# Kernel optimization log

Hardware: AMD Instinct MI355X
Metric: run time of the kernel (lower is better)

The kernel has to match this reference:

```python
import jax, jax.numpy as jnp
import numpy as np

INTERVAL = 0.02

def setup_inputs() -> dict:
    key = jax.random.key(0)
    ks = jax.random.split(key, 10)
    B, N, D, F = 8, 256, 64, 64
    return {
        "rbf_0": jax.random.normal(ks[0], (B, N, N, D), jnp.float32),
        "rbf_d": jax.random.normal(ks[1], (B, N, N, D), jnp.float32),
        "Q0_w": jax.random.normal(ks[2], (F, D), jnp.float32) * 0.1,
        "Q0_b": jax.random.normal(ks[3], (F,), jnp.float32) * 0.1,
        "Q_w": jax.random.normal(ks[4], (F, D), jnp.float32) * 0.1,
        "Q_b": jax.random.normal(ks[5], (F,), jnp.float32) * 0.1,
        "R0_w": jax.random.normal(ks[6], (F, D), jnp.float32) * 0.1,
        "R0_b": jax.random.normal(ks[7], (F,), jnp.float32) * 0.1,
        "R_w": jax.random.normal(ks[8], (F, D), jnp.float32) * 0.1,
        "R_b": jax.random.normal(ks[9], (F,), jnp.float32) * 0.1,
    }

def _linear(x, w, b):
    # x: [..., D], w: [F, D], b: [F] -> [..., F]
    return jnp.einsum('...d,fd->...f', x, w) + b

def reference(rbf_0, rbf_d, Q0_w, Q0_b, Q_w, Q_b, R0_w, R0_b, R_w, R_b):
    q_0 = _linear(rbf_0, Q0_w, Q0_b)   # [B, N, N, F]
    q = _linear(rbf_d, Q_w, Q_b)       # [B, N, N, F]
    r_0 = _linear(rbf_0, R0_w, R0_b)   # [B, N, N, F]
    r = _linear(rbf_d, R_w, R_b)       # [B, N, N, F]
    # 3-index correlator: contract over i and f
    C = jnp.einsum('bnif,bijf->bnj', q_0 * q, r_0 * r) * INTERVAL
    return C
```

## Files before the change

kernel.cpp:

```cpp
#include <hip/hip_runtime.h>
#include <hip/hip_bf16.h>


typedef __bf16 bf16x8 __attribute__((ext_vector_type(8)));
typedef float  f32x4  __attribute__((ext_vector_type(4)));
typedef int    i32x4  __attribute__((ext_vector_type(4)));
typedef unsigned short u16;
typedef u16    u16x8  __attribute__((ext_vector_type(8)));

static __device__ __forceinline__ __bf16 f2bf(float x) {
  union { __hip_bfloat16 h; __bf16 b; } u;
  u.h = __float2bfloat16(x);
  return u.b;
}
static __device__ __forceinline__ u16 f2bfu(float x) {
  union { __hip_bfloat16 h; u16 s; } u;
  u.h = __float2bfloat16(x);
  return u.s;
}
static __device__ __forceinline__ float bfu2f(u16 s) {
  union { unsigned int u; float f; } v;
  v.u = ((unsigned int)s) << 16;
  return v.f;
}
static __device__ __forceinline__ void gload16(const float* gsrc, float* ldst) {
  __builtin_amdgcn_global_load_lds(
      (const __attribute__((address_space(1))) void*)gsrc,
      (__attribute__((address_space(3))) void*)ldst, 16, 0, 0);
}

__global__ __launch_bounds__(256, 3) void k_phase1(
    const float* __restrict__ rbf0, const float* __restrict__ rbfd,
    const float* __restrict__ Q0w, const float* __restrict__ Q0b,
    const float* __restrict__ Qw,  const float* __restrict__ Qb,
    const float* __restrict__ R0w, const float* __restrict__ R0b,
    const float* __restrict__ Rw,  const float* __restrict__ Rb,
    u16* __restrict__ Aout, u16* __restrict__ Bout)
{
  __shared__ __align__(16) float lds[3][2][2048];

  const int tid  = threadIdx.x;
  const int lane = tid & 63;
  const int wave = tid >> 6;
  const int fr   = lane & 15;
  const int kg   = lane >> 4;
  const int role = wave >> 1;
  const int s    = wave & 1;

  const float* W0 = role ? R0w : Q0w;
  const float* W1 = role ? Rw  : Qw;
  const float* B0 = role ? R0b : Q0b;
  const float* B1 = role ? Rb  : Qb;
  u16* __restrict__ Out = role ? Bout : Aout;

  bf16x8 wf0[2][4], wf1[2][4];
#pragma unroll
  for (int kt = 0; kt < 2; ++kt)
#pragma unroll
    for (int ft = 0; ft < 4; ++ft) {
      const float* p0 = W0 + (ft * 16 + fr) * 64 + kt * 32 + kg * 8;
      const float* p1 = W1 + (ft * 16 + fr) * 64 + kt * 32 + kg * 8;
      f32x4 a = *(const f32x4*)p0, b = *(const f32x4*)(p0 + 4);
      f32x4 c = *(const f32x4*)p1, d = *(const f32x4*)(p1 + 4);
      bf16x8 w0v, w1v;
#pragma unroll
      for (int j = 0; j < 4; ++j) {
        w0v[j] = f2bf(a[j]); w0v[j + 4] = f2bf(b[j]);
        w1v[j] = f2bf(c[j]); w1v[j + 4] = f2bf(d[j]);
      }
      wf0[kt][ft] = w0v; wf1[kt][ft] = w1v;
    }

  u16x8 pb0[2], pb1[2];
#pragma unroll
  for (int ft = 0; ft < 4; ++ft)
#pragma unroll
    for (int r = 0; r < 4; ++r) {
      int idx = ft * 4 + r;
      pb0[idx >> 3][idx & 7] = f2bfu(B0[ft * 16 + kg * 4 + r]);
      pb1[idx >> 3][idx & 7] = f2bfu(B1[ft * 16 + kg * 4 + r]);
    }

  const int g0 = tid, g1 = 256 + tid;
  const int c0 = ((g0 >> 4) << 4) | ((g0 & 15) ^ ((g0 >> 4) & 15));
  const int c1 = ((g1 >> 4) << 4) | ((g1 & 15) ^ ((g1 >> 4) & 15));
  const int f0 = c0 * 4, f1 = c1 * 4;
  const int d0 = wave * 256, d1 = (wave + 4) * 256;

  const int bt0 = blockIdx.x;

#define S1_ISSUE(IT, SET)                                              \
  {                                                                    \
    const float* b0_ = rbf0 + (size_t)(bt0 + (IT) * 2048) * 2048;      \
    const float* b1_ = rbfd + (size_t)(bt0 + (IT) * 2048) * 2048;      \
    gload16(b0_ + f0, &lds[SET][0][d0]);                               \
    gload16(b0_ + f1, &lds[SET][0][d1]);                               \
    gload16(b1_ + f0, &lds[SET][1][d0]);                               \
    gload16(b1_ + f1, &lds[SET][1][d1]);                               \
  }

#define S1_COMPUTE(IT, SET)                                            \
  {                                                                    \
    const int row = s * 16 + fr;                     \
    f32x4 ra[4], rb[4];                                                \
    _Pragma("unroll")                                                  \
    for (int kt = 0; kt < 2; ++kt)                                     \
      _Pragma("unroll")                                                \
      for (int h = 0; h < 2; ++h) {                                    \
        int c = kt * 8 + kg * 2 + h;                                   \
        int chunk = (row << 4) | (c ^ fr);                             \
        ra[kt * 2 + h] = *(const f32x4*)&lds[SET][0][chunk * 4];       \
        rb[kt * 2 + h] = *(const f32x4*)&lds[SET][1][chunk * 4];       \
      }                                                                \
    bf16x8 x0f[2], xdf[2];                                             \
    _Pragma("unroll")                                                  \
    for (int kt = 0; kt < 2; ++kt)                                     \
      _Pragma("unroll")                                                \
      for (int j = 0; j < 4; ++j) {                                    \
        x0f[kt][j]     = f2bf(ra[kt * 2][j]);                          \
        x0f[kt][j + 4] = f2bf(ra[kt * 2 + 1][j]);                      \
        xdf[kt][j]     = f2bf(rb[kt * 2][j]);                          \
        xdf[kt][j + 4] = f2bf(rb[kt * 2 + 1][j]);                      \
      }                                                                \
    f32x4 acc0[4], acc1[4];                                            \
    _Pragma("unroll")                                                  \
    for (int ft = 0; ft < 4; ++ft)                                     \
      _Pragma("unroll")                                                \
      for (int r = 0; r < 4; ++r) {                                    \
        int idx = ft * 4 + r;                                          \
        acc0[ft][r] = bfu2f(pb0[idx >> 3][idx & 7]);                   \
        acc1[ft][r] = bfu2f(pb1[idx >> 3][idx & 7]);                   \
      }                                                                \
    _Pragma("unroll")                                                  \
    for (int kt = 0; kt < 2; ++kt)                                     \
      _Pragma("unroll")                                                \
      for (int ft = 0; ft < 4; ++ft) {                                 \
        acc0[ft] = __builtin_amdgcn_mfma_f32_16x16x32_bf16(            \
            wf0[kt][ft], x0f[kt], acc0[ft], 0, 0, 0);                  \
        acc1[ft] = __builtin_amdgcn_mfma_f32_16x16x32_bf16(            \
            wf1[kt][ft], xdf[kt], acc1[ft], 0, 0, 0);                  \
      }                                                                \
    u16x8 o0, o1;                                                      \
    _Pragma("unroll")                                                  \
    for (int ft = 0; ft < 4; ++ft)                                     \
      _Pragma("unroll")                                                \
      for (int r = 0; r < 4; ++r) {                                    \
        int idx = ft * 4 + r;                                          \
        float v = acc0[ft][r] * acc1[ft][r];                           \
        if (idx < 8) o0[idx & 7] = f2bfu(v); else o1[idx & 7] = f2bfu(v); \
      }                                                                \
    u16* dst = Out + ((size_t)((bt0 + (IT) * 2048) * 32 + s * 16 + fr)) * 64 + kg * 16; \
    *(u16x8*)dst       = o0;                                           \
    *(u16x8*)(dst + 8) = o1;                                           \
  }

#define S1_ITER(IT, NWAIT, DO_ISSUE)                                   \
  {                                                                    \
    if (DO_ISSUE) S1_ISSUE((IT) + 2, ((IT) + 2) % 3);                  \
    asm volatile("s_waitcnt vmcnt(" #NWAIT ")" ::: "memory");          \
    __builtin_amdgcn_s_barrier();                                      \
    __builtin_amdgcn_sched_barrier(0);                                 \
    S1_COMPUTE(IT, (IT) % 3);                                          \
    asm volatile("s_waitcnt lgkmcnt(0)" ::: "memory");                 \
    __builtin_amdgcn_s_barrier();                                      \
    __builtin_amdgcn_sched_barrier(0);                                 \
  }

  S1_ISSUE(0, 0);
  S1_ISSUE(1, 1);

  S1_ITER(0,  8, 1);
  S1_ITER(1, 10, 1);
  S1_ITER(2, 12, 1);
  S1_ITER(3, 12, 1);
  S1_ITER(4, 12, 1);
  S1_ITER(5, 12, 1);
  S1_ITER(6,  8, 0);
  S1_ITER(7,  4, 0);

#undef S1_ITER
#undef S1_COMPUTE
#undef S1_ISSUE
}

__global__ __launch_bounds__(256, 2) void k_phase2(
    const u16* __restrict__ A, const u16* __restrict__ Bm,
    float* __restrict__ C)
{
  __shared__ __align__(16) u16 Alds[128 * 64];
  __shared__ __align__(16) u16 Blds[128 * 64];

  const int tid  = threadIdx.x;
  const int lane = tid & 63;
  const int wave = tid >> 6;
  const int fr   = lane & 15;
  const int kg   = lane >> 4;

  const int bid = blockIdx.x;
  const int kc = bid & 15;
  const int jt = (bid >> 4) & 1;
  const int nt = (bid >> 5) & 1;
  const int b  = bid >> 6;
  const int n0 = nt * 128, j0 = jt * 128;
  const int wr = wave >> 1, wc = wave & 1;

  const u16* Ab = A  + (size_t)b * 4194304;
  const u16* Bb = Bm + (size_t)b * 4194304;

  f32x4 acc[4][4];
#pragma unroll
  for (int mt = 0; mt < 4; ++mt)
#pragma unroll
    for (int nn = 0; nn < 4; ++nn) {
      acc[mt][nn][0] = 0.f; acc[mt][nn][1] = 0.f; acc[mt][nn][2] = 0.f; acc[mt][nn][3] = 0.f;
    }

  for (int ii = 0; ii < 16; ++ii) {
    const int i = kc * 16 + ii;

    i32x4 va[4], vb[4];
#pragma unroll
    for (int rep = 0; rep < 4; ++rep) {
      int c = tid + rep * 256;
      int row = c >> 3, ch = c & 7;
      va[rep] = *(const i32x4*)(Ab + (size_t)(n0 + row) * 16384 + (size_t)i * 64 + ch * 8);
      vb[rep] = *(const i32x4*)(Bb + (size_t)i * 16384 + (size_t)(j0 + row) * 64 + ch * 8);
    }
    __syncthreads();
#pragma unroll
    for (int rep = 0; rep < 4; ++rep) {
      int c = tid + rep * 256;
      int row = c >> 3, ch = c & 7;
      int sw = ch ^ (row & 7);
      *(i32x4*)&Alds[row * 64 + sw * 8] = va[rep];
      *(i32x4*)&Blds[row * 64 + sw * 8] = vb[rep];
    }
    __syncthreads();

#pragma unroll
    for (int ks = 0; ks < 2; ++ks) {
      bf16x8 af[4], bfv[4];
#pragma unroll
      for (int mt = 0; mt < 4; ++mt) {
        int row = wr * 64 + mt * 16 + fr;
        int sw = (ks * 4 + kg) ^ (row & 7);
        af[mt] = *(const bf16x8*)&Alds[row * 64 + sw * 8];
      }
#pragma unroll
      for (int nn = 0; nn < 4; ++nn) {
        int row = wc * 64 + nn * 16 + fr;
        int sw = (ks * 4 + kg) ^ (row & 7);
        bfv[nn] = *(const bf16x8*)&Blds[row * 64 + sw * 8];
      }
#pragma unroll
      for (int mt = 0; mt < 4; ++mt)
#pragma unroll
        for (int nn = 0; nn < 4; ++nn)
          acc[mt][nn] = __builtin_amdgcn_mfma_f32_16x16x32_bf16(af[mt], bfv[nn], acc[mt][nn], 0, 0, 0);
    }
  }

  float* Cb = C + ((size_t)b << 16);
#pragma unroll
  for (int mt = 0; mt < 4; ++mt)
#pragma unroll
    for (int nn = 0; nn < 4; ++nn)
#pragma unroll
      for (int r = 0; r < 4; ++r) {
        int n = n0 + wr * 64 + mt * 16 + kg * 4 + r;
        int j = j0 + wc * 64 + nn * 16 + fr;
        atomicAdd(&Cb[n * 256 + j], acc[mt][nn][r] * 0.02f);
      }
}

extern "C" void kernel_launch(void* const* d_in, const int* in_sizes, int n_in,
                              void* d_out, int out_size, void* d_ws, size_t ws_size,
                              hipStream_t stream)
{
  const float* rbf0 = (const float*)d_in[0];
  const float* rbfd = (const float*)d_in[1];
  const float* Q0w  = (const float*)d_in[2];
  const float* Q0b  = (const float*)d_in[3];
  const float* Qw   = (const float*)d_in[4];
  const float* Qb   = (const float*)d_in[5];
  const float* R0w  = (const float*)d_in[6];
  const float* R0b  = (const float*)d_in[7];
  const float* Rw   = (const float*)d_in[8];
  const float* Rb   = (const float*)d_in[9];
  float* out = (float*)d_out;

  u16* Abuf = (u16*)d_ws;
  u16* Bbuf = Abuf + (size_t)33554432;

  hipMemsetAsync(d_out, 0, (size_t)out_size * sizeof(float), stream);
  hipLaunchKernelGGL(k_phase1, dim3(2048), dim3(256), 0, stream,
                     rbf0, rbfd, Q0w, Q0b, Qw, Qb, R0w, R0b, Rw, Rb, Abuf, Bbuf);
  hipLaunchKernelGGL(k_phase2, dim3(512), dim3(256), 0, stream, Abuf, Bbuf, out);
}
```

Measured before the change: 142.1 us.

## Give each wave its own row tile computing all four projections, drop block barriers

Phase 1 now assigns each wave an independent 16-row tile and has it compute all four linear projections (Q0, Q, R0, R) from a per-wave double-buffered LDS staging area. Previously the four waves split the work by role, shared a block-wide triple buffer and needed s_barrier synchronisation. This removes block barriers and lets each wave reuse its loaded rbf tile for both the Q and R products. In exchange every wave holds all four weight sets in registers, which raises register pressure, so occupancy drops to 2 blocks per SIMD and the grid halves to 1024 blocks with shallower prefetch.

Measured after the change: 247.6 us. 1.74x slower.

```diff
diff --git a/kernel.cpp b/kernel.cpp
--- a/kernel.cpp
+++ b/kernel.cpp
@@ -29,7 +29,7 @@
       (__attribute__((address_space(3))) void*)ldst, 16, 0, 0);
 }
 
-__global__ __launch_bounds__(256, 3) void k_phase1(
+__global__ __launch_bounds__(256, 2) void k_phase1(
     const float* __restrict__ rbf0, const float* __restrict__ rbfd,
     const float* __restrict__ Q0w, const float* __restrict__ Q0b,
     const float* __restrict__ Qw,  const float* __restrict__ Qb,
@@ -37,80 +37,79 @@
     const float* __restrict__ Rw,  const float* __restrict__ Rb,
     u16* __restrict__ Aout, u16* __restrict__ Bout)
 {
-  __shared__ __align__(16) float lds[3][2][2048];
+  __shared__ __align__(16) float plds[4][2][2][1024];
 
   const int tid  = threadIdx.x;
   const int lane = tid & 63;
   const int wave = tid >> 6;
   const int fr   = lane & 15;
   const int kg   = lane >> 4;
-  const int role = wave >> 1;
-  const int s    = wave & 1;
-
-  const float* W0 = role ? R0w : Q0w;
-  const float* W1 = role ? Rw  : Qw;
-  const float* B0 = role ? R0b : Q0b;
-  const float* B1 = role ? Rb  : Qb;
-  u16* __restrict__ Out = role ? Bout : Aout;
-
-  bf16x8 wf0[2][4], wf1[2][4];
-#pragma unroll
-  for (int kt = 0; kt < 2; ++kt)
-#pragma unroll
-    for (int ft = 0; ft < 4; ++ft) {
-      const float* p0 = W0 + (ft * 16 + fr) * 64 + kt * 32 + kg * 8;
-      const float* p1 = W1 + (ft * 16 + fr) * 64 + kt * 32 + kg * 8;
-      f32x4 a = *(const f32x4*)p0, b = *(const f32x4*)(p0 + 4);
-      f32x4 c = *(const f32x4*)p1, d = *(const f32x4*)(p1 + 4);
-      bf16x8 w0v, w1v;
-#pragma unroll
-      for (int j = 0; j < 4; ++j) {
-        w0v[j] = f2bf(a[j]); w0v[j + 4] = f2bf(b[j]);
-        w1v[j] = f2bf(c[j]); w1v[j + 4] = f2bf(d[j]);
-      }
-      wf0[kt][ft] = w0v; wf1[kt][ft] = w1v;
-    }
-
-  u16x8 pb0[2], pb1[2];
-#pragma unroll
-  for (int ft = 0; ft < 4; ++ft)
-#pragma unroll
-    for (int r = 0; r < 4; ++r) {
-      int idx = ft * 4 + r;
-      pb0[idx >> 3][idx & 7] = f2bfu(B0[ft * 16 + kg * 4 + r]);
-      pb1[idx >> 3][idx & 7] = f2bfu(B1[ft * 16 + kg * 4 + r]);
-    }
-
-  const int g0 = tid, g1 = 256 + tid;
-  const int c0 = ((g0 >> 4) << 4) | ((g0 & 15) ^ ((g0 >> 4) & 15));
-  const int c1 = ((g1 >> 4) << 4) | ((g1 & 15) ^ ((g1 >> 4) & 15));
-  const int f0 = c0 * 4, f1 = c1 * 4;
-  const int d0 = wave * 256, d1 = (wave + 4) * 256;
-
-  const int bt0 = blockIdx.x;
-
-#define S1_ISSUE(IT, SET)                                              \
+
+  const float* Ws[4] = {Q0w, Qw, R0w, Rw};
+  const float* Bs[4] = {Q0b, Qb, R0b, Rb};
+
+  bf16x8 wf[4][2][4];
+#pragma unroll
+  for (int m = 0; m < 4; ++m)
+#pragma unroll
+    for (int kt = 0; kt < 2; ++kt)
+#pragma unroll
+      for (int ft = 0; ft < 4; ++ft) {
+        const float* p = Ws[m] + (ft * 16 + fr) * 64 + kt * 32 + kg * 8;
+        f32x4 a = *(const f32x4*)p, b = *(const f32x4*)(p + 4);
+        bf16x8 w;
+#pragma unroll
+        for (int j = 0; j < 4; ++j) { w[j] = f2bf(a[j]); w[j + 4] = f2bf(b[j]); }
+        wf[m][kt][ft] = w;
+      }
+
+  u16x8 pb[4][2];
+#pragma unroll
+  for (int m = 0; m < 4; ++m)
+#pragma unroll
+    for (int ft = 0; ft < 4; ++ft)
+#pragma unroll
+      for (int r = 0; r < 4; ++r) {
+        int idx = ft * 4 + r;
+        pb[m][idx >> 3][idx & 7] = f2bfu(Bs[m][ft * 16 + kg * 4 + r]);
+      }
+
+  int sc0, sc1, sc2, sc3;
+  {
+    int g;
+    g = 0 * 64 + lane; sc0 = (((g >> 4) << 4) | ((g & 15) ^ ((g >> 4) & 15))) * 4;
+    g = 1 * 64 + lane; sc1 = (((g >> 4) << 4) | ((g & 15) ^ ((g >> 4) & 15))) * 4;
+    g = 2 * 64 + lane; sc2 = (((g >> 4) << 4) | ((g & 15) ^ ((g >> 4) & 15))) * 4;
+    g = 3 * 64 + lane; sc3 = (((g >> 4) << 4) | ((g & 15) ^ ((g >> 4) & 15))) * 4;
+  }
+
+  const int ws = blockIdx.x * 4 + wave;
+
+#define S1_ISSUE(T, SET)                                               \
   {                                                                    \
-    const float* b0_ = rbf0 + (size_t)(bt0 + (IT) * 2048) * 2048;      \
-    const float* b1_ = rbfd + (size_t)(bt0 + (IT) * 2048) * 2048;      \
-    gload16(b0_ + f0, &lds[SET][0][d0]);                               \
-    gload16(b0_ + f1, &lds[SET][0][d1]);                               \
-    gload16(b1_ + f0, &lds[SET][1][d0]);                               \
-    gload16(b1_ + f1, &lds[SET][1][d1]);                               \
-  }
-
-#define S1_COMPUTE(IT, SET)                                            \
+    const float* b0_ = rbf0 + (size_t)(T) * 1024;                      \
+    const float* b1_ = rbfd + (size_t)(T) * 1024;                      \
+    gload16(b0_ + sc0, &plds[wave][SET][0][0]);                        \
+    gload16(b0_ + sc1, &plds[wave][SET][0][256]);                      \
+    gload16(b0_ + sc2, &plds[wave][SET][0][512]);                      \
+    gload16(b0_ + sc3, &plds[wave][SET][0][768]);                      \
+    gload16(b1_ + sc0, &plds[wave][SET][1][0]);                        \
+    gload16(b1_ + sc1, &plds[wave][SET][1][256]);                      \
+    gload16(b1_ + sc2, &plds[wave][SET][1][512]);                      \
+    gload16(b1_ + sc3, &plds[wave][SET][1][768]);                      \
+  }
+
+#define S1_COMPUTE(T, SET)                                             \
   {                                                                    \
-    const int row = s * 16 + fr;                     \
     f32x4 ra[4], rb[4];                                                \
     _Pragma("unroll")                                                  \
     for (int kt = 0; kt < 2; ++kt)                                     \
       _Pragma("unroll")                                                \
       for (int h = 0; h < 2; ++h) {                                    \
-        int c = kt * 8 + kg * 2 + h;                                   \
-        int chunk = (row << 4) | (c ^ fr);                             \
-        ra[kt * 2 + h] = *(const f32x4*)&lds[SET][0][chunk * 4];       \
-        rb[kt * 2 + h] = *(const f32x4*)&lds[SET][1][chunk * 4];       \
+        int part = kt * 8 + kg * 2 + h;                                \
+        int off = fr * 64 + (part ^ fr) * 4;                           \
+        ra[kt * 2 + h] = *(const f32x4*)&plds[wave][SET][0][off];      \
+        rb[kt * 2 + h] = *(const f32x4*)&plds[wave][SET][1][off];      \
       }                                                                \
     bf16x8 x0f[2], xdf[2];                                             \
     _Pragma("unroll")                                                  \
@@ -122,63 +121,68 @@
         xdf[kt][j]     = f2bf(rb[kt * 2][j]);                          \
         xdf[kt][j + 4] = f2bf(rb[kt * 2 + 1][j]);                      \
       }                                                                \
-    f32x4 acc0[4], acc1[4];                                            \
+    f32x4 acc[4][4];                                                   \
+    _Pragma("unroll")                                                  \
+    for (int m = 0; m < 4; ++m)                                        \
+      _Pragma("unroll")                                                \
+      for (int ft = 0; ft < 4; ++ft)                                   \
+        _Pragma("unroll")                                              \
+        for (int r = 0; r < 4; ++r) {                                  \
+          int idx = ft * 4 + r;                                        \
+          acc[m][ft][r] = bfu2f(pb[m][idx >> 3][idx & 7]);             \
+        }                                                              \
+    _Pragma("unroll")                                                  \
+    for (int kt = 0; kt < 2; ++kt)                                     \
+      _Pragma("unroll")                                                \
+      for (int ft = 0; ft < 4; ++ft) {                                 \
+        acc[0][ft] = __builtin_amdgcn_mfma_f32_16x16x32_bf16(          \
+            wf[0][kt][ft], x0f[kt], acc[0][ft], 0, 0, 0);              \
+        acc[1][ft] = __builtin_amdgcn_mfma_f32_16x16x32_bf16(          \
+            wf[1][kt][ft], xdf[kt], acc[1][ft], 0, 0, 0);              \
+        acc[2][ft] = __builtin_amdgcn_mfma_f32_16x16x32_bf16(          \
+            wf[2][kt][ft], x0f[kt], acc[2][ft], 0, 0, 0);              \
+        acc[3][ft] = __builtin_amdgcn_mfma_f32_16x16x32_bf16(          \
+            wf[3][kt][ft], xdf[kt], acc[3][ft], 0, 0, 0);              \
+      }                                                                \
+    u16x8 oa0, oa1, ob0, ob1;                                          \
     _Pragma("unroll")                                                  \
     for (int ft = 0; ft < 4; ++ft)                                     \
       _Pragma("unroll")                                                \
       for (int r = 0; r < 4; ++r) {                                    \
         int idx = ft * 4 + r;                                          \
-        acc0[ft][r] = bfu2f(pb0[idx >> 3][idx & 7]);                   \
-        acc1[ft][r] = bfu2f(pb1[idx >> 3][idx & 7]);                   \
+        float va = acc[0][ft][r] * acc[1][ft][r];                      \
+        float vb = acc[2][ft][r] * acc[3][ft][r];                      \
+        if (idx < 8) { oa0[idx & 7] = f2bfu(va); ob0[idx & 7] = f2bfu(vb); } \
+        else         { oa1[idx & 7] = f2bfu(va); ob1[idx & 7] = f2bfu(vb); } \
       }                                                                \
-    _Pragma("unroll")                                                  \
-    for (int kt = 0; kt < 2; ++kt)                                     \
-      _Pragma("unroll")                                                \
-      for (int ft = 0; ft < 4; ++ft) {                                 \
-        acc0[ft] = __builtin_amdgcn_mfma_f32_16x16x32_bf16(            \
-            wf0[kt][ft], x0f[kt], acc0[ft], 0, 0, 0);                  \
-        acc1[ft] = __builtin_amdgcn_mfma_f32_16x16x32_bf16(            \
-            wf1[kt][ft], xdf[kt], acc1[ft], 0, 0, 0);                  \
-      }                                                                \
-    u16x8 o0, o1;                                                      \
-    _Pragma("unroll")                                                  \
-    for (int ft = 0; ft < 4; ++ft)                                     \
-      _Pragma("unroll")                                                \
-      for (int r = 0; r < 4; ++r) {                                    \
-        int idx = ft * 4 + r;                                          \
-        float v = acc0[ft][r] * acc1[ft][r];                           \
-        if (idx < 8) o0[idx & 7] = f2bfu(v); else o1[idx & 7] = f2bfu(v); \
-      }                                                                \
-    u16* dst = Out + ((size_t)((bt0 + (IT) * 2048) * 32 + s * 16 + fr)) * 64 + kg * 16; \
-    *(u16x8*)dst       = o0;                                           \
-    *(u16x8*)(dst + 8) = o1;                                           \
-  }
-
-#define S1_ITER(IT, NWAIT, DO_ISSUE)                                   \
+    u16* dstA = Aout + ((size_t)(T) * 16 + fr) * 64 + kg * 16;         \
+    u16* dstB = Bout + ((size_t)(T) * 16 + fr) * 64 + kg * 16;         \
+    *(u16x8*)dstA       = oa0;                                         \
+    *(u16x8*)(dstA + 8) = oa1;                                         \
+    *(u16x8*)dstB       = ob0;                                         \
+    *(u16x8*)(dstB + 8) = ob1;                                         \
+  }
+
+#define S1_STEP(IT, NWAIT, DO_ISSUE)                                   \
   {                                                                    \
-    if (DO_ISSUE) S1_ISSUE((IT) + 2, ((IT) + 2) % 3);                  \
+    if (DO_ISSUE) S1_ISSUE(ws + ((IT) + 1) * 4096, ((IT) + 1) & 1);    \
     asm volatile("s_waitcnt vmcnt(" #NWAIT ")" ::: "memory");          \
-    __builtin_amdgcn_s_barrier();                                      \
     __builtin_amdgcn_sched_barrier(0);                                 \
-    S1_COMPUTE(IT, (IT) % 3);                                          \
-    asm volatile("s_waitcnt lgkmcnt(0)" ::: "memory");                 \
-    __builtin_amdgcn_s_barrier();                                      \
-    __builtin_amdgcn_sched_barrier(0);                                 \
-  }
-
-  S1_ISSUE(0, 0);
-  S1_ISSUE(1, 1);
-
-  S1_ITER(0,  8, 1);
-  S1_ITER(1, 10, 1);
-  S1_ITER(2, 12, 1);
-  S1_ITER(3, 12, 1);
-  S1_ITER(4, 12, 1);
-  S1_ITER(5, 12, 1);
-  S1_ITER(6,  8, 0);
-  S1_ITER(7,  4, 0);
-
-#undef S1_ITER
+    S1_COMPUTE(ws + (IT) * 4096, (IT) & 1);                            \
+  }
+
+  S1_ISSUE(ws, 0);
+
+  S1_STEP(0, 8, 1);
+  S1_STEP(1, 8, 1);
+  S1_STEP(2, 8, 1);
+  S1_STEP(3, 8, 1);
+  S1_STEP(4, 8, 1);
+  S1_STEP(5, 8, 1);
+  S1_STEP(6, 8, 1);
+  S1_STEP(7, 4, 0);
+
+#undef S1_STEP
 #undef S1_COMPUTE
 #undef S1_ISSUE
 }
@@ -212,7 +216,8 @@
   for (int mt = 0; mt < 4; ++mt)
 #pragma unroll
     for (int nn = 0; nn < 4; ++nn) {
-      acc[mt][nn][0] = 0.f; acc[mt][nn][1] = 0.f; acc[mt][nn][2] = 0.f; acc[mt][nn][3] = 0.f;
+      acc[mt][nn][0] = 0.f; acc[mt][nn][1] = 0.f;
+      acc[mt][nn][2] = 0.f; acc[mt][nn][3] = 0.f;
     }
 
   for (int ii = 0; ii < 16; ++ii) {
@@ -293,7 +298,7 @@
   u16* Bbuf = Abuf + (size_t)33554432;
 
   hipMemsetAsync(d_out, 0, (size_t)out_size * sizeof(float), stream);
-  hipLaunchKernelGGL(k_phase1, dim3(2048), dim3(256), 0, stream,
+  hipLaunchKernelGGL(k_phase1, dim3(1024), dim3(256), 0, stream,
                      rbf0, rbfd, Q0w, Q0b, Qw, Qb, R0w, R0b, Rw, Rb, Abuf, Bbuf);
   hipLaunchKernelGGL(k_phase2, dim3(512), dim3(256), 0, stream, Abuf, Bbuf, out);
 }
```
